# Kernel tuning notes

Hardware: AMD Instinct MI355X
Metric: run time of the kernel (lower is better)

The kernel has to match this reference:

```python
import jax, jax.numpy as jnp
import numpy as np
from jax import lax

VOCAB = 504       # vocab_size + 4
EMB = 80
ENC_H = 256       # enc_lstm_dim
DEC_H = 512       # dec_lstm_dim
ATT = 512         # 2*enc_lstm_dim = attention depth = attention_layer_size


def _p(key, shape, scale=0.05):
    return (jax.random.normal(key, shape, dtype=jnp.float32) * scale)


def setup_inputs() -> dict:
    key = jax.random.key(0)
    ks = jax.random.split(key, 24)
    B, H, W = 16, 64, 512
    T = 151
    inp = jax.random.normal(ks[0], (B, H, W, 1), dtype=jnp.float32)
    true_labels = jax.random.randint(ks[1], (B, T), 0, VOCAB)
    d = {
        "inp": inp,
        "true_labels": true_labels,
        "num_words": T,
        # CNN (canonical im2latex stack; init_cnn not in source)
        "ck1": _p(ks[2], (3, 3, 1, 64)),    "cb1": jnp.zeros((64,)),
        "ck2": _p(ks[3], (3, 3, 64, 128)),  "cb2": jnp.zeros((128,)),
        "ck3": _p(ks[4], (3, 3, 128, 256)), "cb3": jnp.zeros((256,)),
        "ck4": _p(ks[5], (3, 3, 256, 512)), "cb4": jnp.zeros((512,)),
        # encoder BiLSTM (input 512, hidden 256), TF LSTMCell layout [in+h, 4h]
        "Wfw": _p(ks[6], (512 + ENC_H, 4 * ENC_H)), "bfw": jnp.zeros((4 * ENC_H,)),
        "Wbw": _p(ks[7], (512 + ENC_H, 4 * ENC_H)), "bbw": jnp.zeros((4 * ENC_H,)),
        # decoder LSTM: input = emb(80) + attention(512) = 592
        "Wdec": _p(ks[8], (EMB + ATT + DEC_H, 4 * DEC_H)), "bdec": jnp.zeros((4 * DEC_H,)),
        # Bahdanau attention
        "Wmem": _p(ks[9], (ATT, ATT)),
        "Wq": _p(ks[10], (DEC_H, ATT)),
        "v_att": _p(ks[11], (ATT,)),
        # AttentionWrapper attention_layer (Dense, no bias)
        "Wattn": _p(ks[12], (DEC_H + ATT, ATT)),
        # output projection
        "Wout": _p(ks[13], (ATT, VOCAB)), "bout": jnp.zeros((VOCAB,)),
        # embedding table
        "embedding": _p(ks[14], (VOCAB, EMB)),
    }
    return d


def _conv(x, k, b):
    y = lax.conv_general_dilated(x, k, (1, 1), 'SAME',
                                 dimension_numbers=('NHWC', 'HWIO', 'NHWC'))
    return jax.nn.relu(y + b)


def _pool(x):
    return lax.reduce_window(x, -jnp.inf, lax.max, (1, 2, 2, 1), (1, 2, 2, 1), 'VALID')


def _run_lstm(xs, W, b, hidden):
    # xs: [T, N, D] time-major; TF LSTMCell: gates i, j, f, o; forget_bias = 1.0
    N = xs.shape[1]
    h0 = jnp.zeros((N, hidden), xs.dtype)
    def step(carry, x):
        h, c = carry
        z = jnp.concatenate([x, h], -1) @ W + b
        i, j, f, o = jnp.split(z, 4, -1)
        c = jax.nn.sigmoid(f + 1.0) * c + jax.nn.sigmoid(i) * jnp.tanh(j)
        h = jax.nn.sigmoid(o) * jnp.tanh(c)
        return (h, c), h
    _, hs = lax.scan(step, (h0, h0), xs)
    return hs  # [T, N, hidden]


def reference(inp, true_labels, num_words,
              ck1, cb1, ck2, cb2, ck3, cb3, ck4, cb4,
              Wfw, bfw, Wbw, bbw, Wdec, bdec,
              Wmem, Wq, v_att, Wattn, Wout, bout, embedding):
    B = inp.shape[0]
    # CNN encoder
    x = _pool(_conv(inp, ck1, cb1))
    x = _pool(_conv(x, ck2, cb2))
    x = _conv(x, ck3, cb3)
    x = _pool(_conv(x, ck4, cb4))            # [B, H', W', 512]
    Hp, Wp, C = x.shape[1], x.shape[2], x.shape[3]
    # per-row BiLSTM (weights shared across rows via tf.make_template)
    rows = x.reshape(B * Hp, Wp, C).transpose(1, 0, 2)   # [W', B*H', C]
    fw = _run_lstm(rows, Wfw, bfw, ENC_H)
    bw = _run_lstm(rows[::-1], Wbw, bbw, ENC_H)[::-1]
    enc = jnp.concatenate([fw, bw], -1)                  # [W', B*H', 512]
    memory = enc.transpose(1, 0, 2).reshape(B, Hp * Wp, ATT)  # [B, L, 512]
    keys = memory @ Wmem                                 # [B, L, 512]

    # decoder with Bahdanau attention, teacher forcing (scheduled sampling
    # prob 0.1 in source treated as pure teacher forcing for determinism)
    T_dec = num_words - 1
    emb_inp = embedding[true_labels[:, :T_dec]]          # [B, T-1, 80]
    emb_tm = emb_inp.transpose(1, 0, 2)                  # [T-1, B, 80]

    h0 = jnp.zeros((B, DEC_H), jnp.float32)
    a0 = jnp.zeros((B, ATT), jnp.float32)

    def step(carry, e):
        h, c, attn = carry
        x_t = jnp.concatenate([e, attn], -1)             # cell_input_fn: concat
        z = jnp.concatenate([x_t, h], -1) @ Wdec + bdec
        i, j, f, o = jnp.split(z, 4, -1)
        c = jax.nn.sigmoid(f + 1.0) * c + jax.nn.sigmoid(i) * jnp.tanh(j)
        h = jax.nn.sigmoid(o) * jnp.tanh(c)
        q = h @ Wq                                       # [B, 512]
        score = jnp.einsum('bld,d->bl', jnp.tanh(keys + q[:, None, :]), v_att)
        align = jax.nn.softmax(score, axis=-1)           # [B, L]
        ctx = jnp.einsum('bl,bld->bd', align, memory)    # [B, 512]
        attn = jnp.concatenate([h, ctx], -1) @ Wattn     # attention_layer, no bias
        logits = attn @ Wout + bout                      # [B, VOCAB]
        return (h, c, attn), logits

    _, logits_tm = lax.scan(step, (h0, h0, a0), emb_tm)  # [T-1, B, V]
    return logits_tm.transpose(1, 0, 2)                  # [B, T-1, V]
```

## Files before the change

### kernel.cpp

```cpp
#include <hip/hip_runtime.h>
#include <cstddef>


#define TDEC 150
#define TLAB 151
typedef unsigned short u16;

__device__ __forceinline__ float sigm(float x) { return 1.0f / (1.0f + __expf(-x)); }
__device__ __forceinline__ float tanhfast(float x) {
  float ax = fabsf(x);
  float e = __expf(-2.0f * ax);
  float t = (1.0f - e) / (1.0f + e);
  return x < 0.0f ? -t : t;
}
__device__ __forceinline__ int EZX(int d) { return ((d & 63) << 3) | (d >> 6); }

__device__ __forceinline__ unsigned ld_cg(const unsigned* p) {
  return __hip_atomic_load(p, __ATOMIC_RELAXED, __HIP_MEMORY_SCOPE_AGENT);
}
__device__ __forceinline__ void st_cg(unsigned* p, unsigned v) {
  __hip_atomic_store(p, v, __ATOMIC_RELAXED, __HIP_MEMORY_SCOPE_AGENT);
}
__device__ __forceinline__ void stf_cg(float* p, float v) {
  __hip_atomic_store(p, v, __ATOMIC_RELAXED, __HIP_MEMORY_SCOPE_AGENT);
}
__device__ __forceinline__ float bfhi(unsigned x) { return __uint_as_float(x & 0xFFFF0000u); }
__device__ __forceinline__ float bflo(unsigned x) { return __uint_as_float(x << 16); }

__global__ __launch_bounds__(256) void conv_pool(
    const float* __restrict__ x, const float* __restrict__ W,
    const float* __restrict__ bias, float* __restrict__ y,
    int Hin, int Win, int Cin, int Cout)
{
  int Hout = Hin >> 1, Wout = Win >> 1;
  int cg = Cout >> 3;
  int idx = blockIdx.x * 256 + threadIdx.x;
  int total = 16 * Hout * Wout * cg;
  if (idx >= total) return;
  int g = idx % cg; int r = idx / cg;
  int pw = r % Wout; r /= Wout;
  int ph = r % Hout; int b = r / Hout;
  int co = g * 8;
  int h0 = ph * 2, w0 = pw * 2;
  float acc[4][8];
#pragma unroll
  for (int p = 0; p < 4; p++)
#pragma unroll
    for (int cc = 0; cc < 8; cc++) acc[p][cc] = 0.0f;
  bool interior = (h0 >= 1) && (h0 + 2 < Hin) && (w0 >= 1) && (w0 + 2 < Win);
  const int rs = Win * Cin;
  for (int ci = 0; ci < Cin; ci++) {
    float patch[4][4];
    if (interior) {
      const float* xp = x + ((b * Hin + (h0 - 1)) * Win + (w0 - 1)) * Cin + ci;
#pragma unroll
      for (int rr = 0; rr < 4; rr++)
#pragma unroll
        for (int cc = 0; cc < 4; cc++)
          patch[rr][cc] = xp[rr * rs + cc * Cin];
    } else {
#pragma unroll
      for (int rr = 0; rr < 4; rr++) {
        int ih = h0 - 1 + rr;
#pragma unroll
        for (int cc = 0; cc < 4; cc++) {
          int iw = w0 - 1 + cc;
          patch[rr][cc] = (ih >= 0 && ih < Hin && iw >= 0 && iw < Win)
                              ? x[((b * Hin + ih) * Win + iw) * Cin + ci] : 0.0f;
        }
      }
    }
#pragma unroll
    for (int ky = 0; ky < 3; ky++) {
#pragma unroll
      for (int kx = 0; kx < 3; kx++) {
        const float* wp = W + (((ky * 3 + kx) * Cin) + ci) * Cout + co;
        float4 wa = *(const float4*)wp;
        float4 wb = *(const float4*)(wp + 4);
        float w8[8] = {wa.x, wa.y, wa.z, wa.w, wb.x, wb.y, wb.z, wb.w};
#pragma unroll
        for (int py = 0; py < 2; py++)
#pragma unroll
          for (int px = 0; px < 2; px++) {
            float iv = patch[py + ky][px + kx];
#pragma unroll
            for (int cc = 0; cc < 8; cc++) acc[py * 2 + px][cc] += iv * w8[cc];
          }
      }
    }
  }
  float* yp = y + ((b * Hout + ph) * Wout + pw) * Cout + co;
#pragma unroll
  for (int cc = 0; cc < 8; cc++) {
    float m = fmaxf(fmaxf(acc[0][cc], acc[1][cc]), fmaxf(acc[2][cc], acc[3][cc]));
    yp[cc] = fmaxf(m + bias[co + cc], 0.0f);
  }
}

__global__ __launch_bounds__(256) void conv_pool2(
    const float* __restrict__ x, const float* __restrict__ W,
    const float* __restrict__ bias, float* __restrict__ y,
    int Hin, int Win, int Cin, int Cout)
{
  int Hout = Hin >> 1, Wout = Win >> 1, Wq2 = Wout >> 1;
  int cg = Cout >> 3;
  int idx = blockIdx.x * 256 + threadIdx.x;
  int total = 16 * Hout * Wq2 * cg;
  if (idx >= total) return;
  int g = idx % cg; int r = idx / cg;
  int wq = r % Wq2; r /= Wq2;
  int ph = r % Hout; int b = r / Hout;
  int co = g * 8;
  int h0 = ph * 2, w0 = wq * 4;
  float acc[8][8];
#pragma unroll
  for (int p = 0; p < 8; p++)
#pragma unroll
    for (int cc = 0; cc < 8; cc++) acc[p][cc] = 0.0f;
  bool interior = (h0 >= 1) && (h0 + 2 < Hin) && (w0 >= 1) && (w0 + 4 < Win);
  const int rs = Win * Cin;
  for (int ci = 0; ci < Cin; ci++) {
    float patch[4][6];
    if (interior) {
      const float* xp = x + ((b * Hin + (h0 - 1)) * Win + (w0 - 1)) * Cin + ci;
#pragma unroll
      for (int rr = 0; rr < 4; rr++)
#pragma unroll
        for (int cc = 0; cc < 6; cc++)
          patch[rr][cc] = xp[rr * rs + cc * Cin];
    } else {
#pragma unroll
      for (int rr = 0; rr < 4; rr++) {
        int ih = h0 - 1 + rr;
#pragma unroll
        for (int cc = 0; cc < 6; cc++) {
          int iw = w0 - 1 + cc;
          patch[rr][cc] = (ih >= 0 && ih < Hin && iw >= 0 && iw < Win)
                              ? x[((b * Hin + ih) * Win + iw) * Cin + ci] : 0.0f;
        }
      }
    }
#pragma unroll
    for (int ky = 0; ky < 3; ky++) {
#pragma unroll
      for (int kx = 0; kx < 3; kx++) {
        const float* wp = W + (((ky * 3 + kx) * Cin) + ci) * Cout + co;
        float4 wa = *(const float4*)wp;
        float4 wb = *(const float4*)(wp + 4);
        float w8[8] = {wa.x, wa.y, wa.z, wa.w, wb.x, wb.y, wb.z, wb.w};
#pragma unroll
        for (int px0 = 0; px0 < 2; px0++)
#pragma unroll
          for (int py = 0; py < 2; py++)
#pragma unroll
            for (int px = 0; px < 2; px++) {
              float iv = patch[py + ky][px0 * 2 + px + kx];
              int ap = px0 * 4 + py * 2 + px;
#pragma unroll
              for (int cc = 0; cc < 8; cc++) acc[ap][cc] += iv * w8[cc];
            }
      }
    }
  }
#pragma unroll
  for (int px0 = 0; px0 < 2; px0++) {
    float* yp = y + ((b * Hout + ph) * Wout + wq * 2 + px0) * Cout + co;
#pragma unroll
    for (int cc = 0; cc < 8; cc++) {
      float m = fmaxf(fmaxf(acc[px0 * 4 + 0][cc], acc[px0 * 4 + 1][cc]),
                      fmaxf(acc[px0 * 4 + 2][cc], acc[px0 * 4 + 3][cc]));
      yp[cc] = fmaxf(m + bias[co + cc], 0.0f);
    }
  }
}

__global__ __launch_bounds__(256) void conv_nopool2(
    const float* __restrict__ x, const float* __restrict__ W,
    const float* __restrict__ bias, float* __restrict__ y,
    int H, int Wd, int Cin, int Cout)
{
  int Wd2 = Wd >> 1;
  int cg = Cout >> 3;
  int idx = blockIdx.x * 256 + threadIdx.x;
  int total = 16 * H * Wd2 * cg;
  if (idx >= total) return;
  int g = idx % cg; int r = idx / cg;
  int wq = r % Wd2; r /= Wd2;
  int h = r % H; int b = r / H;
  int co = g * 8;
  int w0 = wq * 2;
  float acc[2][8];
#pragma unroll
  for (int p = 0; p < 2; p++)
#pragma unroll
    for (int cc = 0; cc < 8; cc++) acc[p][cc] = 0.0f;
  bool interior = (h >= 1) && (h + 1 < H) && (w0 >= 1) && (w0 + 2 < Wd);
  const int rs = Wd * Cin;
  for (int ci = 0; ci < Cin; ci++) {
    float patch[3][4];
    if (interior) {
      const float* xp = x + ((b * H + (h - 1)) * Wd + (w0 - 1)) * Cin + ci;
#pragma unroll
      for (int rr = 0; rr < 3; rr++)
#pragma unroll
        for (int cc = 0; cc < 4; cc++)
          patch[rr][cc] = xp[rr * rs + cc * Cin];
    } else {
#pragma unroll
      for (int rr = 0; rr < 3; rr++) {
        int ih = h - 1 + rr;
#pragma unroll
        for (int cc = 0; cc < 4; cc++) {
          int iw = w0 - 1 + cc;
          patch[rr][cc] = (ih >= 0 && ih < H && iw >= 0 && iw < Wd)
                              ? x[((b * H + ih) * Wd + iw) * Cin + ci] : 0.0f;
        }
      }
    }
#pragma unroll
    for (int ky = 0; ky < 3; ky++) {
#pragma unroll
      for (int kx = 0; kx < 3; kx++) {
        const float* wp = W + (((ky * 3 + kx) * Cin) + ci) * Cout + co;
        float4 wa = *(const float4*)wp;
        float4 wb = *(const float4*)(wp + 4);
        float w8[8] = {wa.x, wa.y, wa.z, wa.w, wb.x, wb.y, wb.z, wb.w};
#pragma unroll
        for (int px = 0; px < 2; px++) {
          float iv = patch[ky][px + kx];
#pragma unroll
          for (int cc = 0; cc < 8; cc++) acc[px][cc] += iv * w8[cc];
        }
      }
    }
  }
#pragma unroll
  for (int px = 0; px < 2; px++) {
    float* yp = y + ((b * H + h) * Wd + w0 + px) * Cout + co;
#pragma unroll
    for (int cc = 0; cc < 8; cc++)
      yp[cc] = fmaxf(acc[px][cc] + bias[co + cc], 0.0f);
  }
}

__global__ __launch_bounds__(256) void sgemm128(
    const float* __restrict__ A, int lda,
    const float* __restrict__ Bm, int ldb,
    void* __restrict__ C, int ldc,
    const float* __restrict__ bias,
    const float* __restrict__ Dadd, int ldd,
    int M, int N, int K, int amode, int cmode,
    const int* __restrict__ labels, const float* __restrict__ emb)
{
  __shared__ float As[8][132];
  __shared__ float Bs[8][132];
  int tid = threadIdx.x;
  int m0 = blockIdx.y * 128, n0 = blockIdx.x * 128;
  int tx = tid & 15, ty = tid >> 4;
  float acc[8][8];
#pragma unroll
  for (int i = 0; i < 8; i++)
#pragma unroll
    for (int j = 0; j < 8; j++) acc[i][j] = 0.0f;
  int arow = tid >> 1, ak = (tid & 1) * 4;
  int bkr = tid >> 5, bn = (tid & 31) * 4;
  for (int k0 = 0; k0 < K; k0 += 8) {
    float4 av = make_float4(0.f, 0.f, 0.f, 0.f);
    int row = m0 + arow;
    if (row < M) {
      const float* ap;
      if (amode == 0) {
        ap = A + (size_t)row * lda + k0 + ak;
      } else {
        int t = row >> 4, b = row & 15;
        ap = emb + labels[b * TLAB + t] * 80 + k0 + ak;
      }
      av = *(const float4*)ap;
    }
    As[ak + 0][arow] = av.x; As[ak + 1][arow] = av.y;
    As[ak + 2][arow] = av.z; As[ak + 3][arow] = av.w;
    {
      float4 bv = make_float4(0.f, 0.f, 0.f, 0.f);
      int col = n0 + bn;
      const float* bp = Bm + (size_t)(k0 + bkr) * ldb + col;
      if (col + 3 < N) {
        bv = *(const float4*)bp;
      } else if (col < N) {
        bv.x = bp[0];
        if (col + 1 < N) bv.y = bp[1];
        if (col + 2 < N) bv.z = bp[2];
      }
      *(float4*)&Bs[bkr][bn] = bv;
    }
    __syncthreads();
#pragma unroll
    for (int kk = 0; kk < 8; kk++) {
      float a[8], b[8];
      *(float4*)&a[0] = *(const float4*)&As[kk][ty * 8];
      *(float4*)&a[4] = *(const float4*)&As[kk][ty * 8 + 4];
      *(float4*)&b[0] = *(const float4*)&Bs[kk][tx * 8];
      *(float4*)&b[4] = *(const float4*)&Bs[kk][tx * 8 + 4];
#pragma unroll
      for (int i = 0; i < 8; i++)
#pragma unroll
        for (int j = 0; j < 8; j++) acc[i][j] += a[i] * b[j];
    }
    __syncthreads();
  }
#pragma unroll
  for (int i = 0; i < 8; i++) {
    int row = m0 + ty * 8 + i;
    if (row >= M) continue;
#pragma unroll
    for (int j = 0; j < 8; j++) {
      int col = n0 + tx * 8 + j;
      if (col >= N) continue;
      float v = acc[i][j];
      if (Dadd) v += Dadd[(size_t)row * ldd + col];
      if (bias) v += bias[col];
      if (cmode == 0) {
        ((float*)C)[(size_t)row * ldc + col] = v;
      } else if (cmode == 1) {
        int t = row >> 4, b2 = row & 15;
        ((float*)C)[((size_t)b2 * TDEC + t) * 504 + col] = v;
      } else if (cmode == 2) {
        ((float*)C)[(size_t)col * ldc + row] = v;
      } else if (cmode == 3) {
        unsigned bits = __float_as_uint(v);
        u16 h = (u16)((bits + 0x8000u) >> 16);
        ((u16*)C)[(size_t)row * ldc + col] = h;
      } else {
        int b2 = row >> 9, l = row & 511;
        unsigned bits = __float_as_uint(v);
        u16 h = (u16)((bits + 0x8000u) >> 16);
        ((u16*)C)[((size_t)(b2 * 512 + col)) * 512 + l] = h;
      }
    }
  }
}

__global__ __launch_bounds__(256) void transpose32(
    const float* __restrict__ src, int lds_, int M, int N,
    float* __restrict__ dst, int ldd_, int off)
{
  __shared__ float tle[32][33];
  int tid = threadIdx.x;
  int x = tid & 31, y8 = tid >> 5;
  int m0 = blockIdx.y * 32, n0 = blockIdx.x * 32;
#pragma unroll
  for (int p = 0; p < 4; p++) {
    int m = m0 + y8 + p * 8, n = n0 + x;
    if (m < M && n < N) tle[y8 + p * 8][x] = src[(size_t)m * lds_ + n];
  }
  __syncthreads();
#pragma unroll
  for (int p = 0; p < 4; p++) {
    int n = n0 + y8 + p * 8, m = m0 + x;
    if (n < N && m < M) dst[(size_t)n * ldd_ + off + m] = tle[x][y8 + p * 8];
  }
}

__global__ __launch_bounds__(256) void enc_step2(
    const float* __restrict__ Zfw, const float* __restrict__ Zbw,
    const float* __restrict__ Whfw, const float* __restrict__ Whbw,
    const float* __restrict__ hin, float* __restrict__ hout,
    float* __restrict__ cst, float* __restrict__ mem, int t)
{
  __shared__ float WL[16][260];
  __shared__ float zl[128][17];
  int tid = threadIdx.x;
  int bi = blockIdx.x;
  int dir = bi >> 6;
  int u0 = (bi & 63) * 4;
  const float* Wh = dir ? Whbw : Whfw;
  const float* Z = dir ? Zbw : Zfw;
  int wp = dir ? (63 - t) : t;
  {
    const float* src = Wh + (size_t)tid * 1024 + u0;
#pragma unroll
    for (int g = 0; g < 4; g++) {
      float4 w4 = *(const float4*)(src + g * 256);
      WL[g * 4 + 0][tid] = w4.x; WL[g * 4 + 1][tid] = w4.y;
      WL[g * 4 + 2][tid] = w4.z; WL[g * 4 + 3][tid] = w4.w;
    }
  }
  __syncthreads();
  {
    int c2 = tid & 7, q = tid >> 3;
    const float* hb = hin + dir * 32768 + q * 4 * 256;
    float acc[4][2];
#pragma unroll
    for (int i = 0; i < 4; i++) { acc[i][0] = 0.f; acc[i][1] = 0.f; }
    for (int k4 = 0; k4 < 64; k4++) {
      float4 w0 = *(const float4*)&WL[c2 * 2 + 0][k4 * 4];
      float4 w1 = *(const float4*)&WL[c2 * 2 + 1][k4 * 4];
#pragma unroll
      for (int i = 0; i < 4; i++) {
        float4 h4 = *(const float4*)&hb[i * 256 + k4 * 4];
        acc[i][0] += h4.x * w0.x + h4.y * w0.y + h4.z * w0.z + h4.w * w0.w;
        acc[i][1] += h4.x * w1.x + h4.y * w1.y + h4.z * w1.z + h4.w * w1.w;
      }
    }
#pragma unroll
    for (int i = 0; i < 4; i++) {
      zl[q * 4 + i][c2 * 2 + 0] = acc[i][0];
      zl[q * 4 + i][c2 * 2 + 1] = acc[i][1];
    }
  }
  __syncthreads();
#pragma unroll
  for (int s2 = 0; s2 < 2; s2++) {
    int s = tid + s2 * 256;
    int n = s >> 2, uj = s & 3;
    int u = u0 + uj;
    size_t zoff = ((size_t)(n * 64 + wp)) * 1024 + u;
    float zi = zl[n][0 + uj] + Z[zoff];
    float zj = zl[n][4 + uj] + Z[zoff + 256];
    float zf = zl[n][8 + uj] + Z[zoff + 512];
    float zo = zl[n][12 + uj] + Z[zoff + 768];
    int ci = dir * 32768 + n * 256 + u;
    float cold = cst[ci];
    float cn = sigm(zf + 1.0f) * cold + sigm(zi) * tanhfast(zj);
    float hn = sigm(zo) * tanhfast(cn);
    cst[ci] = cn;
    hout[ci] = hn;
    int b = n >> 3, hp = n & 7;
    mem[((size_t)(b * 512 + hp * 64 + wp)) * 512 + dir * 256 + u] = hn;
  }
}

__device__ __forceinline__ void bar_full(unsigned* arr, unsigned* gar,
                                         unsigned* relx, unsigned ep) {
  asm volatile("s_waitcnt vmcnt(0)" ::: "memory");
  __syncthreads();
  int tid = threadIdx.x;
  int bi = blockIdx.x;
  int xcd = bi & 7;
  if (tid == 0) st_cg(&arr[bi * 32], ep);
  if (bi < 8) {
    if (tid < 32)
      while (ld_cg(&arr[(xcd + tid * 8) * 32]) < ep) __builtin_amdgcn_s_sleep(2);
    __syncthreads();
    if (tid == 0) st_cg(&gar[xcd * 32], ep);
    if (tid < 8)
      while (ld_cg(&gar[tid * 32]) < ep) __builtin_amdgcn_s_sleep(2);
    __syncthreads();
    if (tid == 0) st_cg(&relx[xcd * 32], ep);
  } else {
    if (tid == 0)
      while (ld_cg(&relx[xcd * 32]) < ep) __builtin_amdgcn_s_sleep(2);
  }
  __syncthreads();
  asm volatile("" ::: "memory");
}
__device__ __forceinline__ void bar_grp(unsigned* arr, int g, unsigned ep) {
  asm volatile("s_waitcnt vmcnt(0)" ::: "memory");
  __syncthreads();
  int tid = threadIdx.x;
  if (tid == 0) st_cg(&arr[blockIdx.x * 32], ep);
  if (tid < 16) {
    int peer = (g & 7) + ((g >> 3) << 7) + (tid << 3);
    while (ld_cg(&arr[peer * 32]) < ep) __builtin_amdgcn_s_sleep(2);
  }
  __syncthreads();
  asm volatile("" ::: "memory");
}

__global__ __launch_bounds__(256) void dec_persist(
    const float* __restrict__ WcatT, const float* __restrict__ Zemb,
    const float* __restrict__ WqT, const u16* __restrict__ keysB,
    const u16* __restrict__ memBT, const float* __restrict__ vatt,
    float* __restrict__ hist, float* __restrict__ qbuf_t,
    float* __restrict__ scor_t, unsigned* __restrict__ arr,
    unsigned* __restrict__ gar, unsigned* __restrict__ relx)
{
  __shared__ float hl[16][516];
  __shared__ unsigned WTB[8][524];
  __shared__ float vbs[512];
  __shared__ float ez[512];
  __shared__ float red[256];
  __shared__ float zl[16][8];
  __shared__ float cstL[16][2];
  int tid = threadIdx.x;
  int bi = blockIdx.x;
  int bq = (bi & 7) + 8 * (bi >> 7);
  int chunk = (bi >> 3) & 15;

  {
    int c = tid >> 5, lt = tid & 31;
    int u = bi * 2 + (c & 1), g = c >> 1;
    const float* srcw = WcatT + ((size_t)(g * 512 + u)) * 1024;
#pragma unroll
    for (int i = 0; i < 16; i++) {
      int kk = lt + 32 * i;
      unsigned b0 = (__float_as_uint(srcw[kk * 2]) + 0x8000u) >> 16;
      unsigned b1 = (__float_as_uint(srcw[kk * 2 + 1]) + 0x8000u) & 0xFFFF0000u;
      WTB[c][kk] = b0 | b1;
    }
  }
  if (tid < 128) {
    float4 v4 = ((const float4*)vatt)[tid];
    int d = tid * 4;
    vbs[EZX(d + 0)] = v4.x; vbs[EZX(d + 1)] = v4.y;
    vbs[EZX(d + 2)] = v4.z; vbs[EZX(d + 3)] = v4.w;
  }
  if (tid < 32) cstL[tid >> 1][tid & 1] = 0.0f;
  __syncthreads();

  for (int t = 0; t < TDEC; t++) {
    {
      float acc = 0.0f;
      int b = tid >> 4, c = (tid >> 1) & 7, ks = tid & 1;
      if (t > 0) {
        const float* hp = hist + (size_t)(t - 1) * 16384;
#pragma unroll
        for (int half = 0; half < 2; half++) {
          __syncthreads();
#pragma unroll
          for (int it = 0; it < 8; it++) {
            int f4 = it * 256 + tid;
            int sb = f4 >> 7, si = (f4 & 127) * 4;
            *(float4*)&hl[sb][si] = *(const float4*)&hp[sb * 1024 + half * 512 + si];
          }
          __syncthreads();
          const unsigned* wrow = &WTB[c][half * 256 + ks * 128];
          const float* hrow = &hl[b][ks * 256];
#pragma unroll 8
          for (int i = 0; i < 32; i++) {
            uint4 wv = *(const uint4*)&wrow[i * 4];
            float4 h0 = *(const float4*)&hrow[i * 8];
            float4 h1 = *(const float4*)&hrow[i * 8 + 4];
            acc += bflo(wv.x) * h0.x + bfhi(wv.x) * h0.y
                 + bflo(wv.y) * h0.z + bfhi(wv.y) * h0.w
                 + bflo(wv.z) * h1.x + bfhi(wv.z) * h1.y
                 + bflo(wv.w) * h1.z + bfhi(wv.w) * h1.w;
          }
        }
      }
      acc += __shfl_xor(acc, 1, 64);
      if (ks == 0) {
        int u = bi * 2 + (c & 1), g = c >> 1;
        zl[b][c] = acc + Zemb[(size_t)(t * 16 + b) * 2048 + g * 512 + u];
      }
    }
    __syncthreads();
    if (tid < 32) {
      int b = tid >> 1, uu = tid & 1;
      float zi = zl[b][uu], zj = zl[b][2 + uu], zf = zl[b][4 + uu], zo = zl[b][6 + uu];
      float cold = cstL[b][uu];
      float cn = sigm(zf + 1.0f) * cold + sigm(zi) * tanhfast(zj);
      float hn = sigm(zo) * tanhfast(cn);
      cstL[b][uu] = cn;
      stf_cg(&hist[(size_t)t * 16384 + b * 1024 + bi * 2 + uu], hn);
    }
    bar_full(arr, gar, relx, 4 * t + 1);

    {
      int jl = tid >> 3, ks = tid & 7;
      int j = chunk * 32 + jl;
      const float* wr = WqT + (size_t)j * 512 + ks * 64;
      const float* hr = hist + (size_t)t * 16384 + bq * 1024 + ks * 64;
      float acc = 0.f;
#pragma unroll
      for (int i = 0; i < 16; i++) {
        float4 w4 = *(const float4*)&wr[i * 4];
        float4 h4 = *(const float4*)&hr[i * 4];
        acc += w4.x * h4.x + w4.y * h4.y + w4.z * h4.z + w4.w * h4.w;
      }
      acc += __shfl_xor(acc, 1, 64);
      acc += __shfl_xor(acc, 2, 64);
      acc += __shfl_xor(acc, 4, 64);
      if (ks == 0) stf_cg(&qbuf_t[(size_t)t * 8192 + bq * 512 + j], acc);
    }
    bar_grp(arr, bq, 4 * t + 2);

    {
      int l = chunk * 32 + (tid >> 3), dk = tid & 7;
      const u16* kp = keysB + ((size_t)(bq * 512 + l)) * 512 + dk * 64;
      const float* qp = qbuf_t + (size_t)t * 8192 + bq * 512 + dk * 64;
      float acc = 0.f;
#pragma unroll
      for (int i = 0; i < 8; i++) {
        uint4 kv = *(const uint4*)(kp + i * 8);
        float4 qa = *(const float4*)(qp + i * 8);
        float4 qb = *(const float4*)(qp + i * 8 + 4);
        int base = i * 64 + dk;
        acc += vbs[base +  0] * tanhfast(bflo(kv.x) + qa.x);
        acc += vbs[base +  8] * tanhfast(bfhi(kv.x) + qa.y);
        acc += vbs[base + 16] * tanhfast(bflo(kv.y) + qa.z);
        acc += vbs[base + 24] * tanhfast(bfhi(kv.y) + qa.w);
        acc += vbs[base + 32] * tanhfast(bflo(kv.z) + qb.x);
        acc += vbs[base + 40] * tanhfast(bfhi(kv.z) + qb.y);
        acc += vbs[base + 48] * tanhfast(bflo(kv.w) + qb.z);
        acc += vbs[base + 56] * tanhfast(bfhi(kv.w) + qb.w);
      }
      acc += __shfl_xor(acc, 1, 64);
      acc += __shfl_xor(acc, 2, 64);
      acc += __shfl_xor(acc, 4, 64);
      if (dk == 0) stf_cg(&scor_t[(size_t)t * 8192 + bq * 512 + l], acc);
    }
    bar_grp(arr, bq, 4 * t + 3);

    {
      float2 sv = *(const float2*)&scor_t[(size_t)t * 8192 + bq * 512 + tid * 2];
      float e0 = __expf(sv.x), e1 = __expf(sv.y);
      ez[EZX(tid * 2)] = e0; ez[EZX(tid * 2 + 1)] = e1;
      red[tid] = e0 + e1;
      __syncthreads();
      for (int s = 128; s > 0; s >>= 1) {
        if (tid < s) red[tid] += red[tid + s];
        __syncthreads();
      }
      float den = red[0];
      int jl = tid >> 3, ls = tid & 7;
      int j = chunk * 32 + jl;
      const u16* mp = memBT + ((size_t)(bq * 512 + j)) * 512 + ls * 64;
      float acc = 0.f;
#pragma unroll
      for (int i = 0; i < 8; i++) {
        uint4 mv = *(const uint4*)(mp + i * 8);
        int base = i * 64 + ls;
        acc += ez[base +  0] * bflo(mv.x);
        acc += ez[base +  8] * bfhi(mv.x);
        acc += ez[base + 16] * bflo(mv.y);
        acc += ez[base + 24] * bfhi(mv.y);
        acc += ez[base + 32] * bflo(mv.z);
        acc += ez[base + 40] * bfhi(mv.z);
        acc += ez[base + 48] * bflo(mv.w);
        acc += ez[base + 56] * bfhi(mv.w);
      }
      acc += __shfl_xor(acc, 1, 64);
      acc += __shfl_xor(acc, 2, 64);
      acc += __shfl_xor(acc, 4, 64);
      if (ls == 0)
        stf_cg(&hist[(size_t)t * 16384 + bq * 1024 + 512 + j], acc / den);
    }
    bar_full(arr, gar, relx, 4 * t + 4);
  }
}

extern "C" void kernel_launch(void* const* d_in, const int* in_sizes, int n_in,
                              void* d_out, int out_size, void* d_ws, size_t ws_size,
                              hipStream_t stream) {
  (void)in_sizes; (void)n_in; (void)out_size; (void)ws_size;
  const float* inp   = (const float*)d_in[0];
  const int*   labels= (const int*)  d_in[1];
  const float* ck1 = (const float*)d_in[3];
  const float* cb1 = (const float*)d_in[4];
  const float* ck2 = (const float*)d_in[5];
  const float* cb2 = (const float*)d_in[6];
  const float* ck3 = (const float*)d_in[7];
  const float* cb3 = (const float*)d_in[8];
  const float* ck4 = (const float*)d_in[9];
  const float* cb4 = (const float*)d_in[10];
  const float* Wfw = (const float*)d_in[11];
  const float* bfw = (const float*)d_in[12];
  const float* Wbw = (const float*)d_in[13];
  const float* bbw = (const float*)d_in[14];
  const float* Wdec= (const float*)d_in[15];
  const float* bdec= (const float*)d_in[16];
  const float* Wmem= (const float*)d_in[17];
  const float* Wq  = (const float*)d_in[18];
  const float* vatt= (const float*)d_in[19];
  const float* Wattn=(const float*)d_in[20];
  const float* Wout= (const float*)d_in[21];
  const float* bout= (const float*)d_in[22];
  const float* emb = (const float*)d_in[23];
  float* out = (float*)d_out;
  float* ws  = (float*)d_ws;

  const size_t OFF_P1    = 0;
  const size_t OFF_ZBW   = 8388608;
  const size_t OFF_QT    = 8388608;
  const size_t OFF_ST    = 9617408;
  const size_t OFF_C3    = 12582912;
  const size_t OFF_HIST  = 16777216;
  const size_t OFF_P4    = 20971520;
  const size_t OFF_MEM   = 25165824;
  const size_t OFF_KEYSB = 29360128;
  const size_t OFF_MEMBT = 31457280;
  const size_t OFF_WCATT = 33554432;
  const size_t OFF_WQT   = 35651584;
  const size_t OFF_WCAT2 = 35913728;
  const size_t OFF_HA    = 36429824;
  const size_t OFF_HB    = 36495360;
  const size_t OFF_CENC  = 36560896;
  const size_t OFF_ARR   = 36626432;
  const size_t OFF_GAR   = 36634624;
  const size_t OFF_RELX  = 36634880;

  float* p1    = ws + OFF_P1;
  float* p2    = ws + OFF_ZBW;
  float* c3    = ws + OFF_C3;
  float* p4    = ws + OFF_P4;
  float* Zfw   = ws + OFF_P1;
  float* Zbw   = ws + OFF_ZBW;
  float* Zemb  = ws + OFF_P1;
  float* qbuf_t= ws + OFF_QT;
  float* scor_t= ws + OFF_ST;
  float* hist  = ws + OFF_HIST;
  float* memv  = ws + OFF_MEM;
  u16*   keysB = (u16*)(ws + OFF_KEYSB);
  u16*   memBT = (u16*)(ws + OFF_MEMBT);
  float* WcatT = ws + OFF_WCATT;
  float* WqT   = ws + OFF_WQT;
  float* Wcat2 = ws + OFF_WCAT2;
  float* hA    = ws + OFF_HA;
  float* hB    = ws + OFF_HB;
  float* cenc  = ws + OFF_CENC;
  unsigned* arr = (unsigned*)(ws + OFF_ARR);
  unsigned* gar = (unsigned*)(ws + OFF_GAR);
  unsigned* relx= (unsigned*)(ws + OFF_RELX);

  hipMemsetAsync(hA,   0, 65536 * 4, stream);
  hipMemsetAsync(cenc, 0, 65536 * 4, stream);
  hipMemsetAsync(arr,  0, (8192 + 512) * 4, stream);

  conv_pool   <<<4096, 256, 0, stream>>>(inp, ck1, cb1, p1, 64, 512, 1, 64);
  conv_pool2  <<<1024, 256, 0, stream>>>(p1, ck2, cb2, p2, 32, 256, 64, 128);
  conv_nopool2<<<2048, 256, 0, stream>>>(p2, ck3, cb3, c3, 16, 128, 128, 256);
  conv_pool2  <<<1024, 256, 0, stream>>>(c3, ck4, cb4, p4, 16, 128, 256, 512);

  sgemm128<<<dim3(8, 64), 256, 0, stream>>>(p4, 512, Wfw, 1024, Zfw, 1024, bfw,
                                            nullptr, 0, 8192, 1024, 512, 0, 0, nullptr, nullptr);
  sgemm128<<<dim3(8, 64), 256, 0, stream>>>(p4, 512, Wbw, 1024, Zbw, 1024, bbw,
                                            nullptr, 0, 8192, 1024, 512, 0, 0, nullptr, nullptr);
  for (int t = 0; t < 64; t++) {
    const float* hin = (t & 1) ? hB : hA;
    float* hout = (t & 1) ? hA : hB;
    enc_step2<<<128, 256, 0, stream>>>(Zfw, Zbw, Wfw + 512 * 1024, Wbw + 512 * 1024,
                                       hin, hout, cenc, memv, t);
  }

  sgemm128<<<dim3(4, 64), 256, 0, stream>>>(memv, 512, Wmem, 512, keysB, 512,
                                            nullptr, nullptr, 0, 8192, 512, 512, 0, 3, nullptr, nullptr);
  sgemm128<<<dim3(4, 64), 256, 0, stream>>>(memv, 512, Wattn + 512 * 512, 512, memBT, 512,
                                            nullptr, nullptr, 0, 8192, 512, 512, 0, 4, nullptr, nullptr);
  sgemm128<<<dim3(16, 4), 256, 0, stream>>>(Wattn, 512, Wdec + 80 * 2048, 2048, WcatT, 1024,
                                            nullptr, Wdec + 592 * 2048, 2048,
                                            512, 2048, 512, 0, 2, nullptr, nullptr);
  transpose32<<<dim3(64, 16), 256, 0, stream>>>(Wdec + 80 * 2048, 2048, 512, 2048, WcatT, 1024, 512);
  transpose32<<<dim3(16, 16), 256, 0, stream>>>(Wq, 512, 512, 512, WqT, 512, 0);
  sgemm128<<<dim3(4, 4), 256, 0, stream>>>(Wattn, 512, Wout, 504, Wcat2, 504,
                                           nullptr, nullptr, 0, 512, 504, 512, 0, 0, nullptr, nullptr);
  hipMemcpyAsync(Wcat2 + 512 * 504, Wout, (size_t)512 * 504 * 4, hipMemcpyDeviceToDevice, stream);
  sgemm128<<<dim3(16, 19), 256, 0, stream>>>(nullptr, 0, Wdec, 2048, Zemb, 2048, bdec,
                                             nullptr, 0, 2400, 2048, 80, 1, 0, labels, emb);

  dec_persist<<<256, 256, 0, stream>>>(WcatT, Zemb, WqT, keysB, memBT, vatt,
                                       hist, qbuf_t, scor_t, arr, gar, relx);

  sgemm128<<<dim3(4, 19), 256, 0, stream>>>(hist, 1024, Wcat2, 504, out, 504, bout,
                                            nullptr, 0, 2400, 504, 1024, 0, 1, nullptr, nullptr);
}
```

Baseline: 8.632 ms.

## Make encoder LSTM persistent, flatten decoder barrier, use fp32 weights and shuffle reductions

Replaces the 64 per-timestep encoder launches with one persistent kernel that keeps cell state in registers and synchronises blocks through a global flag barrier, with h history stored in a workspace buffer. The decoder's hierarchical three-level grid barrier becomes a flat barrier where all threads poll, and acquire fences are added. The decoder recurrent weights go from bf16-packed to fp32 in LDS, and the softmax denominator reduction uses wave shuffles instead of a tree in shared memory. The aim is to cut launch overhead and barrier latency. The trade-offs are more LDS use, heavier polling traffic on the flat barrier, and a reliance on all 128 encoder blocks being co-resident.

```diff
diff --git a/kernel.cpp b/kernel.cpp
--- a/kernel.cpp
+++ b/kernel.cpp
@@ -23,6 +23,9 @@
 }
 __device__ __forceinline__ void stf_cg(float* p, float v) {
   __hip_atomic_store(p, v, __ATOMIC_RELAXED, __HIP_MEMORY_SCOPE_AGENT);
+}
+__device__ __forceinline__ void acq_fence() {
+  __builtin_amdgcn_fence(__ATOMIC_ACQUIRE, "agent");
 }
 __device__ __forceinline__ float bfhi(unsigned x) { return __uint_as_float(x & 0xFFFF0000u); }
 __device__ __forceinline__ float bflo(unsigned x) { return __uint_as_float(x << 16); }
@@ -360,21 +363,20 @@
   }
 }
 
-__global__ __launch_bounds__(256) void enc_step2(
+__global__ __launch_bounds__(256) void enc_persist(
     const float* __restrict__ Zfw, const float* __restrict__ Zbw,
     const float* __restrict__ Whfw, const float* __restrict__ Whbw,
-    const float* __restrict__ hin, float* __restrict__ hout,
-    float* __restrict__ cst, float* __restrict__ mem, int t)
+    float* __restrict__ henc, float* __restrict__ mem,
+    unsigned* __restrict__ earr)
 {
   __shared__ float WL[16][260];
+  __shared__ float hsh[128][130];
   __shared__ float zl[128][17];
   int tid = threadIdx.x;
   int bi = blockIdx.x;
-  int dir = bi >> 6;
-  int u0 = (bi & 63) * 4;
+  int dir = bi >> 6, u0 = (bi & 63) * 4;
   const float* Wh = dir ? Whbw : Whfw;
   const float* Z = dir ? Zbw : Zfw;
-  int wp = dir ? (63 - t) : t;
   {
     const float* src = Wh + (size_t)tid * 1024 + u0;
 #pragma unroll
@@ -384,74 +386,84 @@
       WL[g * 4 + 2][tid] = w4.z; WL[g * 4 + 3][tid] = w4.w;
     }
   }
+  float creg[2] = {0.0f, 0.0f};
   __syncthreads();
-  {
-    int c2 = tid & 7, q = tid >> 3;
-    const float* hb = hin + dir * 32768 + q * 4 * 256;
-    float acc[4][2];
-#pragma unroll
-    for (int i = 0; i < 4; i++) { acc[i][0] = 0.f; acc[i][1] = 0.f; }
-    for (int k4 = 0; k4 < 64; k4++) {
-      float4 w0 = *(const float4*)&WL[c2 * 2 + 0][k4 * 4];
-      float4 w1 = *(const float4*)&WL[c2 * 2 + 1][k4 * 4];
-#pragma unroll
-      for (int i = 0; i < 4; i++) {
-        float4 h4 = *(const float4*)&hb[i * 256 + k4 * 4];
-        acc[i][0] += h4.x * w0.x + h4.y * w0.y + h4.z * w0.z + h4.w * w0.w;
-        acc[i][1] += h4.x * w1.x + h4.y * w1.y + h4.z * w1.z + h4.w * w1.w;
+
+  int c2 = tid & 7, q = tid >> 3;
+  for (int t = 0; t < 64; t++) {
+    int wp = dir ? (63 - t) : t;
+    float a0[4], a1[4];
+#pragma unroll
+    for (int i = 0; i < 4; i++) { a0[i] = 0.f; a1[i] = 0.f; }
+    if (t > 0) {
+      const float* hsrc = henc + (size_t)t * 65536 + dir * 32768;
+#pragma unroll
+      for (int half = 0; half < 2; half++) {
+        __syncthreads();
+#pragma unroll
+        for (int i = 0; i < 16; i++) {
+          int flat = i * 256 + tid;
+          int n = flat >> 5, kq = flat & 31;
+          *(float4*)&hsh[n][kq * 4] = *(const float4*)&hsrc[n * 256 + half * 128 + kq * 4];
+        }
+        __syncthreads();
+        int kw = half * 128;
+        for (int k4 = 0; k4 < 32; k4++) {
+          float4 w0 = *(const float4*)&WL[c2 * 2 + 0][kw + k4 * 4];
+          float4 w1 = *(const float4*)&WL[c2 * 2 + 1][kw + k4 * 4];
+#pragma unroll
+          for (int i = 0; i < 4; i++) {
+            float4 h4 = *(const float4*)&hsh[q * 4 + i][k4 * 4];
+            a0[i] += h4.x * w0.x + h4.y * w0.y + h4.z * w0.z + h4.w * w0.w;
+            a1[i] += h4.x * w1.x + h4.y * w1.y + h4.z * w1.z + h4.w * w1.w;
+          }
+        }
       }
     }
 #pragma unroll
     for (int i = 0; i < 4; i++) {
-      zl[q * 4 + i][c2 * 2 + 0] = acc[i][0];
-      zl[q * 4 + i][c2 * 2 + 1] = acc[i][1];
-    }
-  }
-  __syncthreads();
-#pragma unroll
-  for (int s2 = 0; s2 < 2; s2++) {
-    int s = tid + s2 * 256;
-    int n = s >> 2, uj = s & 3;
-    int u = u0 + uj;
-    size_t zoff = ((size_t)(n * 64 + wp)) * 1024 + u;
-    float zi = zl[n][0 + uj] + Z[zoff];
-    float zj = zl[n][4 + uj] + Z[zoff + 256];
-    float zf = zl[n][8 + uj] + Z[zoff + 512];
-    float zo = zl[n][12 + uj] + Z[zoff + 768];
-    int ci = dir * 32768 + n * 256 + u;
-    float cold = cst[ci];
-    float cn = sigm(zf + 1.0f) * cold + sigm(zi) * tanhfast(zj);
-    float hn = sigm(zo) * tanhfast(cn);
-    cst[ci] = cn;
-    hout[ci] = hn;
-    int b = n >> 3, hp = n & 7;
-    mem[((size_t)(b * 512 + hp * 64 + wp)) * 512 + dir * 256 + u] = hn;
-  }
-}
-
-__device__ __forceinline__ void bar_full(unsigned* arr, unsigned* gar,
-                                         unsigned* relx, unsigned ep) {
+      zl[q * 4 + i][c2 * 2 + 0] = a0[i];
+      zl[q * 4 + i][c2 * 2 + 1] = a1[i];
+    }
+    __syncthreads();
+#pragma unroll
+    for (int s2 = 0; s2 < 2; s2++) {
+      int s = tid + s2 * 256;
+      int n = s >> 2, uj = s & 3;
+      int u = u0 + uj;
+      size_t zoff = ((size_t)(n * 64 + wp)) * 1024 + u;
+      float zi = zl[n][0 + uj] + Z[zoff];
+      float zj = zl[n][4 + uj] + Z[zoff + 256];
+      float zf = zl[n][8 + uj] + Z[zoff + 512];
+      float zo = zl[n][12 + uj] + Z[zoff + 768];
+      float cn = sigm(zf + 1.0f) * creg[s2] + sigm(zi) * tanhfast(zj);
+      float hn = sigm(zo) * tanhfast(cn);
+      creg[s2] = cn;
+      if (t < 63)
+        stf_cg(&henc[(size_t)(t + 1) * 65536 + dir * 32768 + n * 256 + u], hn);
+      int b = n >> 3, hp = n & 7;
+      mem[((size_t)(b * 512 + hp * 64 + wp)) * 512 + dir * 256 + u] = hn;
+    }
+    if (t < 63) {
+      asm volatile("s_waitcnt vmcnt(0)" ::: "memory");
+      __syncthreads();
+      unsigned ep = t + 1;
+      if (tid == 0) st_cg(&earr[bi * 32], ep);
+      if (tid < 128)
+        while (ld_cg(&earr[tid * 32]) < ep) __builtin_amdgcn_s_sleep(2);
+      __syncthreads();
+      acq_fence();
+    }
+  }
+}
+
+__device__ __forceinline__ void bar_full(unsigned* arr, unsigned ep) {
   asm volatile("s_waitcnt vmcnt(0)" ::: "memory");
   __syncthreads();
-  int tid = threadIdx.x;
-  int bi = blockIdx.x;
-  int xcd = bi & 7;
-  if (tid == 0) st_cg(&arr[bi * 32], ep);
-  if (bi < 8) {
-    if (tid < 32)
-      while (ld_cg(&arr[(xcd + tid * 8) * 32]) < ep) __builtin_amdgcn_s_sleep(2);
-    __syncthreads();
-    if (tid == 0) st_cg(&gar[xcd * 32], ep);
-    if (tid < 8)
-      while (ld_cg(&gar[tid * 32]) < ep) __builtin_amdgcn_s_sleep(2);
-    __syncthreads();
-    if (tid == 0) st_cg(&relx[xcd * 32], ep);
-  } else {
-    if (tid == 0)
-      while (ld_cg(&relx[xcd * 32]) < ep) __builtin_amdgcn_s_sleep(2);
-  }
+  if (threadIdx.x == 0) st_cg(&arr[blockIdx.x * 32], ep);
+  while (ld_cg(&arr[threadIdx.x * 32]) < ep) __builtin_amdgcn_s_sleep(2);
   __syncthreads();
-  asm volatile("" ::: "memory");
+  acq_fence();
 }
 __device__ __forceinline__ void bar_grp(unsigned* arr, int g, unsigned ep) {
   asm volatile("s_waitcnt vmcnt(0)" ::: "memory");
@@ -463,7 +475,7 @@
     while (ld_cg(&arr[peer * 32]) < ep) __builtin_amdgcn_s_sleep(2);
   }
   __syncthreads();
-  asm volatile("" ::: "memory");
+  acq_fence();
 }
 
 __global__ __launch_bounds__(256) void dec_persist(
@@ -471,14 +483,13 @@
     const float* __restrict__ WqT, const u16* __restrict__ keysB,
     const u16* __restrict__ memBT, const float* __restrict__ vatt,
     float* __restrict__ hist, float* __restrict__ qbuf_t,
-    float* __restrict__ scor_t, unsigned* __restrict__ arr,
-    unsigned* __restrict__ gar, unsigned* __restrict__ relx)
+    float* __restrict__ scor_t, unsigned* __restrict__ arr)
 {
   __shared__ float hl[16][516];
-  __shared__ unsigned WTB[8][524];
+  __shared__ float WT[8][1036];
   __shared__ float vbs[512];
   __shared__ float ez[512];
-  __shared__ float red[256];
+  __shared__ float redw[4];
   __shared__ float zl[16][8];
   __shared__ float cstL[16][2];
   int tid = threadIdx.x;
@@ -491,11 +502,9 @@
     int u = bi * 2 + (c & 1), g = c >> 1;
     const float* srcw = WcatT + ((size_t)(g * 512 + u)) * 1024;
 #pragma unroll
-    for (int i = 0; i < 16; i++) {
-      int kk = lt + 32 * i;
-      unsigned b0 = (__float_as_uint(srcw[kk * 2]) + 0x8000u) >> 16;
-      unsigned b1 = (__float_as_uint(srcw[kk * 2 + 1]) + 0x8000u) & 0xFFFF0000u;
-      WTB[c][kk] = b0 | b1;
+    for (int i = 0; i < 8; i++) {
+      int k = i * 128 + lt * 4;
+      *(float4*)&WT[c][k] = *(const float4*)&srcw[k];
     }
   }
   if (tid < 128) {
@@ -523,17 +532,13 @@
             *(float4*)&hl[sb][si] = *(const float4*)&hp[sb * 1024 + half * 512 + si];
           }
           __syncthreads();
-          const unsigned* wrow = &WTB[c][half * 256 + ks * 128];
+          const float* wrow = &WT[c][half * 512 + ks * 256];
           const float* hrow = &hl[b][ks * 256];
 #pragma unroll 8
-          for (int i = 0; i < 32; i++) {
-            uint4 wv = *(const uint4*)&wrow[i * 4];
-            float4 h0 = *(const float4*)&hrow[i * 8];
-            float4 h1 = *(const float4*)&hrow[i * 8 + 4];
-            acc += bflo(wv.x) * h0.x + bfhi(wv.x) * h0.y
-                 + bflo(wv.y) * h0.z + bfhi(wv.y) * h0.w
-                 + bflo(wv.z) * h1.x + bfhi(wv.z) * h1.y
-                 + bflo(wv.w) * h1.z + bfhi(wv.w) * h1.w;
+          for (int i = 0; i < 64; i++) {
+            float4 w4 = *(const float4*)&wrow[i * 4];
+            float4 h4 = *(const float4*)&hrow[i * 4];
+            acc += w4.x * h4.x + w4.y * h4.y + w4.z * h4.z + w4.w * h4.w;
           }
         }
       }
@@ -553,7 +558,7 @@
       cstL[b][uu] = cn;
       stf_cg(&hist[(size_t)t * 16384 + b * 1024 + bi * 2 + uu], hn);
     }
-    bar_full(arr, gar, relx, 4 * t + 1);
+    bar_full(arr, 4 * t + 1);
 
     {
       int jl = tid >> 3, ks = tid & 7;
@@ -605,13 +610,12 @@
       float2 sv = *(const float2*)&scor_t[(size_t)t * 8192 + bq * 512 + tid * 2];
       float e0 = __expf(sv.x), e1 = __expf(sv.y);
       ez[EZX(tid * 2)] = e0; ez[EZX(tid * 2 + 1)] = e1;
-      red[tid] = e0 + e1;
+      float s = e0 + e1;
+#pragma unroll
+      for (int d = 1; d < 64; d <<= 1) s += __shfl_xor(s, d, 64);
+      if ((tid & 63) == 0) redw[tid >> 6] = s;
       __syncthreads();
-      for (int s = 128; s > 0; s >>= 1) {
-        if (tid < s) red[tid] += red[tid + s];
-        __syncthreads();
-      }
-      float den = red[0];
+      float den = redw[0] + redw[1] + redw[2] + redw[3];
       int jl = tid >> 3, ls = tid & 7;
       int j = chunk * 32 + jl;
       const u16* mp = memBT + ((size_t)(bq * 512 + j)) * 512 + ls * 64;
@@ -635,7 +639,7 @@
       if (ls == 0)
         stf_cg(&hist[(size_t)t * 16384 + bq * 1024 + 512 + j], acc / den);
     }
-    bar_full(arr, gar, relx, 4 * t + 4);
+    if (t < TDEC - 1) bar_full(arr, 4 * t + 4);
   }
 }
 
@@ -682,12 +686,8 @@
   const size_t OFF_WCATT = 33554432;
   const size_t OFF_WQT   = 35651584;
   const size_t OFF_WCAT2 = 35913728;
-  const size_t OFF_HA    = 36429824;
-  const size_t OFF_HB    = 36495360;
-  const size_t OFF_CENC  = 36560896;
-  const size_t OFF_ARR   = 36626432;
-  const size_t OFF_GAR   = 36634624;
-  const size_t OFF_RELX  = 36634880;
+  const size_t OFF_ARR   = 36429824;
+  const size_t OFF_EARR  = 36438016;
 
   float* p1    = ws + OFF_P1;
   float* p2    = ws + OFF_ZBW;
@@ -699,22 +699,17 @@
   float* qbuf_t= ws + OFF_QT;
   float* scor_t= ws + OFF_ST;
   float* hist  = ws + OFF_HIST;
+  float* henc  = ws + OFF_HIST;
   float* memv  = ws + OFF_MEM;
   u16*   keysB = (u16*)(ws + OFF_KEYSB);
   u16*   memBT = (u16*)(ws + OFF_MEMBT);
   float* WcatT = ws + OFF_WCATT;
   float* WqT   = ws + OFF_WQT;
   float* Wcat2 = ws + OFF_WCAT2;
-  float* hA    = ws + OFF_HA;
-  float* hB    = ws + OFF_HB;
-  float* cenc  = ws + OFF_CENC;
-  unsigned* arr = (unsigned*)(ws + OFF_ARR);
-  unsigned* gar = (unsigned*)(ws + OFF_GAR);
-  unsigned* relx= (unsigned*)(ws + OFF_RELX);
-
-  hipMemsetAsync(hA,   0, 65536 * 4, stream);
-  hipMemsetAsync(cenc, 0, 65536 * 4, stream);
-  hipMemsetAsync(arr,  0, (8192 + 512) * 4, stream);
+  unsigned* arr  = (unsigned*)(ws + OFF_ARR);
+  unsigned* earr = (unsigned*)(ws + OFF_EARR);
+
+  hipMemsetAsync(arr, 0, (8192 + 4096) * 4, stream);
 
   conv_pool   <<<4096, 256, 0, stream>>>(inp, ck1, cb1, p1, 64, 512, 1, 64);
   conv_pool2  <<<1024, 256, 0, stream>>>(p1, ck2, cb2, p2, 32, 256, 64, 128);
@@ -725,12 +720,8 @@
                                             nullptr, 0, 8192, 1024, 512, 0, 0, nullptr, nullptr);
   sgemm128<<<dim3(8, 64), 256, 0, stream>>>(p4, 512, Wbw, 1024, Zbw, 1024, bbw,
                                             nullptr, 0, 8192, 1024, 512, 0, 0, nullptr, nullptr);
-  for (int t = 0; t < 64; t++) {
-    const float* hin = (t & 1) ? hB : hA;
-    float* hout = (t & 1) ? hA : hB;
-    enc_step2<<<128, 256, 0, stream>>>(Zfw, Zbw, Wfw + 512 * 1024, Wbw + 512 * 1024,
-                                       hin, hout, cenc, memv, t);
-  }
+  enc_persist<<<128, 256, 0, stream>>>(Zfw, Zbw, Wfw + 512 * 1024, Wbw + 512 * 1024,
+                                       henc, memv, earr);
 
   sgemm128<<<dim3(4, 64), 256, 0, stream>>>(memv, 512, Wmem, 512, keysB, 512,
                                             nullptr, nullptr, 0, 8192, 512, 512, 0, 3, nullptr, nullptr);
@@ -748,7 +739,7 @@
                                              nullptr, 0, 2400, 2048, 80, 1, 0, labels, emb);
 
   dec_persist<<<256, 256, 0, stream>>>(WcatT, Zemb, WqT, keysB, memBT, vatt,
-                                       hist, qbuf_t, scor_t, arr, gar, relx);
+                                       hist, qbuf_t, scor_t, arr);
 
   sgemm128<<<dim3(4, 19), 256, 0, stream>>>(hist, 1024, Wcat2, 504, out, 504, bout,
                                             nullptr, 0, 2400, 504, 1024, 0, 1, nullptr, nullptr);
```

Result: slower. 12.56 ms (+45.5%).
